# Kernel optimization log

Hardware: AMD Instinct MI355X
Metric: run time of the kernel (lower is better)

## Reference

```python
import jax, jax.numpy as jnp
import numpy as np

H = 2048        # hidden_size
NH = 16         # num heads
QLR = 1536      # q_lora_rank
KVLR = 512      # kv_lora_rank
NOPE = 128      # qk_nope_head_dim
ROPE = 64       # qk_rope_head_dim
VH = 128        # v_head_dim
QHD = NOPE + ROPE
EPS = 1e-6
THETA = 10000.0


def rms_norm(x, w):
    x32 = x.astype(jnp.float32)
    inv = jax.lax.rsqrt(jnp.mean(x32 * x32, axis=-1, keepdims=True) + EPS)
    return (x32 * inv * w.astype(jnp.float32)).astype(x.dtype)


def rotate_half(x):
    h = x.shape[-1] // 2
    return jnp.concatenate([-x[..., h:], x[..., :h]], axis=-1)


def setup_inputs() -> dict:
    key = jax.random.key(0)
    ks = jax.random.split(key, 8)
    s = 0.02
    return {
        "hidden_states": jax.random.normal(ks[0], (1, 2048, H), dtype=jnp.float32),
        "q_a_w": jax.random.normal(ks[1], (QLR, H), dtype=jnp.float32) * s,
        "q_a_ln_w": jnp.ones((QLR,), dtype=jnp.float32),
        "q_b_w": jax.random.normal(ks[2], (NH * QHD, QLR), dtype=jnp.float32) * s,
        "kv_a_w": jax.random.normal(ks[3], (KVLR + ROPE, H), dtype=jnp.float32) * s,
        "kv_a_ln_w": jnp.ones((KVLR,), dtype=jnp.float32),
        "kv_b_w": jax.random.normal(ks[4], (NH * (NOPE + VH), KVLR), dtype=jnp.float32) * s,
        "o_w": jax.random.normal(ks[5], (H, NH * VH), dtype=jnp.float32) * s,
    }


def reference(hidden_states, q_a_w, q_a_ln_w, q_b_w, kv_a_w, kv_a_ln_w, kv_b_w, o_w):
    bsz, q_len, _ = hidden_states.shape
    scale = QHD ** -0.5

    # Q path: low-rank down-proj -> RMSNorm -> up-proj
    q_lat = rms_norm(hidden_states @ q_a_w.T, q_a_ln_w)
    q = (q_lat @ q_b_w.T).reshape(bsz, q_len, NH, QHD).transpose(0, 2, 1, 3)  # [B,H,S,QHD]
    q_nope, q_pe = q[..., :NOPE], q[..., NOPE:]

    # KV path: shared latent + decoupled rope key
    kv_lat_pe = hidden_states @ kv_a_w.T
    kv_lat, k_pe = kv_lat_pe[..., :KVLR], kv_lat_pe[..., KVLR:]
    k_pe = k_pe.reshape(bsz, q_len, 1, ROPE).transpose(0, 2, 1, 3)  # [B,1,S,R]
    kv = (rms_norm(kv_lat, kv_a_ln_w) @ kv_b_w.T).reshape(bsz, q_len, NH, NOPE + VH).transpose(0, 2, 1, 3)
    k_nope, v = kv[..., :NOPE], kv[..., NOPE:]

    # RoPE on decoupled sub-dim
    inv_freq = 1.0 / THETA ** (jnp.arange(0, ROPE, 2, dtype=jnp.float32) / ROPE)
    t = jnp.arange(q_len, dtype=jnp.float32)
    freqs = jnp.outer(t, inv_freq)
    emb = jnp.concatenate([freqs, freqs], axis=-1)
    cos = jnp.cos(emb)[None, None]  # [1,1,S,R]
    sin = jnp.sin(emb)[None, None]
    q_pe = q_pe * cos + rotate_half(q_pe) * sin
    k_pe = k_pe * cos + rotate_half(k_pe) * sin

    qs = jnp.concatenate([q_nope, q_pe], axis=-1)                                   # [B,H,S,QHD]
    ks = jnp.concatenate([k_nope, jnp.broadcast_to(k_pe, (bsz, NH, q_len, ROPE))], axis=-1)

    # causal SDPA
    scores = jnp.einsum('bhqd,bhkd->bhqk', qs, ks) * scale
    mask = jnp.tril(jnp.ones((q_len, q_len), dtype=bool))
    scores = jnp.where(mask[None, None], scores, jnp.finfo(scores.dtype).min)
    p = jax.nn.softmax(scores, axis=-1)
    attn = jnp.einsum('bhqk,bhkd->bhqd', p, v)

    attn = attn.transpose(0, 2, 1, 3).reshape(bsz, q_len, NH * VH)
    return attn @ o_w.T
```

## Files before the change

kernel.cpp:

```cpp
#include <hip/hip_runtime.h>
#include <cstdint>

#define H 2048
#define NH 16
#define QLR 1536
#define KVLR 512
#define NOPE 128
#define ROPED 64
#define VH 128
#define QHD 192
#define SEQ 2048
#define NQH (NH*QHD)
#define NKVC (NH*(NOPE+VH))
#define NOV (NH*VH)
#define KVAW_N (KVLR+ROPED)
#define SCALE_L2E 0.10411755f
#define NSEG 4

typedef __attribute__((ext_vector_type(8))) short short8;
typedef __attribute__((ext_vector_type(4))) short short4v;
typedef __attribute__((ext_vector_type(4))) float floatx4;

__device__ __forceinline__ short f2bf(float x) {
  unsigned u = __builtin_bit_cast(unsigned, x);
  unsigned r = (u + 0x7FFFu + ((u >> 16) & 1u)) >> 16;
  return (short)(unsigned short)r;
}
__device__ __forceinline__ float bf2f(short s) {
  unsigned u = ((unsigned)(unsigned short)s) << 16;
  return __builtin_bit_cast(float, u);
}
__device__ __forceinline__ void g2l16(const void* g, void* l) {
  __builtin_amdgcn_global_load_lds(
      (const __attribute__((address_space(1))) void*)(uintptr_t)(g),
      (__attribute__((address_space(3))) void*)(uintptr_t)(l),
      16, 0, 0);
}


struct CvtArgs {
  const float* src[6];
  short* dst[6];
  int cum[7];
};
__global__ __launch_bounds__(256) void k_cvt_all(CvtArgs a, int total4) {
  int stride = gridDim.x * 256;
  for (int i = blockIdx.x * 256 + threadIdx.x; i < total4; i += stride) {
    int j = 0;
#pragma unroll
    for (int t = 1; t < 6; ++t) j += (i >= a.cum[t]);
    int loc = i - a.cum[j];
    float4 v = ((const float4*)a.src[j])[loc];
    short4v o;
    o.x = f2bf(v.x); o.y = f2bf(v.y); o.z = f2bf(v.z); o.w = f2bf(v.w);
    ((short4v*)a.dst[j])[loc] = o;
  }
}

template<int EPI>
__global__ __launch_bounds__(256) void k_gemm64(
    const short* __restrict__ A, const short* __restrict__ B,
    float* __restrict__ C, float* __restrict__ C2, int N, int K)
{
  __shared__ short As[3][4096];
  __shared__ short Bs[3][2048];
  const int tid = threadIdx.x;
  const int lane = tid & 63;
  const int w = tid >> 6;
  const int wm = w & 1, wn = w >> 1;
  const int quad = lane >> 4, l16 = lane & 15;
  const int m0 = blockIdx.x * 128, n0 = blockIdx.y * 64;
  const int T = K >> 5;

  floatx4 acc[4][2] = {};

  auto issue = [&](int t, int buf) {
#pragma unroll
    for (int i = 0; i < 2; ++i) {
      int c = i*256 + tid;
      int row = c & 127, koct = c >> 7;
      g2l16(A + (size_t)(m0 + row)*K + t*32 + koct*8, As[buf] + (koct*128 + row)*8);
    }
    { int c = tid; int row = c & 63, koct = c >> 6;
      g2l16(B + (size_t)(n0 + row)*K + t*32 + koct*8, Bs[buf] + (koct*64 + row)*8); }
  };

  issue(0, 0);
  issue(1, 1);
  int buf = 0;
  for (int t = 0; t < T; ++t) {
    if (t + 2 < T) {
      int nb = buf - 1; if (nb < 0) nb = 2;
      issue(t + 2, nb);
      asm volatile("s_waitcnt vmcnt(6)" ::: "memory");
    } else if (t + 1 < T) {
      asm volatile("s_waitcnt vmcnt(3)" ::: "memory");
    } else {
      asm volatile("s_waitcnt vmcnt(0)" ::: "memory");
    }
    asm volatile("s_barrier" ::: "memory");
    short8 af[4], bfr[2];
#pragma unroll
    for (int mi = 0; mi < 4; ++mi)
      af[mi] = *(const short8*)(As[buf] + (quad*128 + wm*64 + mi*16 + l16)*8);
#pragma unroll
    for (int ni = 0; ni < 2; ++ni)
      bfr[ni] = *(const short8*)(Bs[buf] + (quad*64 + wn*32 + ni*16 + l16)*8);
#pragma unroll
    for (int mi = 0; mi < 4; ++mi)
#pragma unroll
      for (int ni = 0; ni < 2; ++ni)
        acc[mi][ni] = __builtin_amdgcn_mfma_f32_16x16x32_bf16(af[mi], bfr[ni], acc[mi][ni], 0, 0, 0);
    asm volatile("s_barrier" ::: "memory");
    buf = buf + 1; if (buf > 2) buf = 0;
  }

#pragma unroll
  for (int mi = 0; mi < 4; ++mi) {
#pragma unroll
    for (int ni = 0; ni < 2; ++ni) {
      int col = n0 + wn*32 + ni*16 + l16;
#pragma unroll
      for (int r = 0; r < 4; ++r) {
        int row = m0 + wm*64 + mi*16 + quad*4 + r;
        if (EPI == 0) {
          C[(size_t)row*N + col] = acc[mi][ni][r];
        } else {
          if (col < QLR) C[(size_t)row*QLR + col] = acc[mi][ni][r];
          else           C2[(size_t)row*KVAW_N + (col - QLR)] = acc[mi][ni][r];
        }
      }
    }
  }
}

__global__ __launch_bounds__(256) void k_gemm2(
    const short* __restrict__ qlatn, const short* __restrict__ qbw,
    const short* __restrict__ kvln,  const short* __restrict__ kvbw,
    short* __restrict__ qhm, short* __restrict__ knope, short* __restrict__ vTd)
{
  __shared__ short As[3][4096];
  __shared__ short Bs[3][4096];
  const int tid = threadIdx.x;
  const int lane = tid & 63;
  const int w = tid >> 6;
  const int wm = w & 1, wn = w >> 1;
  const int quad = lane >> 4, l16 = lane & 15;
  int bid = blockIdx.x;
  const short *A, *B; int K, m0, n0; bool isq;
  if (bid < 384) { isq = true;  A = qlatn; B = qbw;  K = QLR;
    m0 = (bid & 15) * 128; n0 = (bid >> 4) * 128; }
  else { int b2 = bid - 384; isq = false; A = kvln; B = kvbw; K = KVLR;
    m0 = (b2 & 15) * 128; n0 = (b2 >> 4) * 128; }
  const int T = K >> 5;

  floatx4 acc[4][4] = {};

  auto issue = [&](int t, int buf) {
#pragma unroll
    for (int i = 0; i < 2; ++i) {
      int c = i*256 + tid;
      int row = c & 127, koct = c >> 7;
      g2l16(A + (size_t)(m0 + row)*K + t*32 + koct*8, As[buf] + (koct*128 + row)*8);
      g2l16(B + (size_t)(n0 + row)*K + t*32 + koct*8, Bs[buf] + (koct*128 + row)*8);
    }
  };

  issue(0, 0);
  issue(1, 1);
  int buf = 0;
  for (int t = 0; t < T; ++t) {
    if (t + 2 < T) {
      int nb = buf - 1; if (nb < 0) nb = 2;
      issue(t + 2, nb);
      asm volatile("s_waitcnt vmcnt(8)" ::: "memory");
    } else if (t + 1 < T) {
      asm volatile("s_waitcnt vmcnt(4)" ::: "memory");
    } else {
      asm volatile("s_waitcnt vmcnt(0)" ::: "memory");
    }
    asm volatile("s_barrier" ::: "memory");
    short8 af[4], bfr[4];
#pragma unroll
    for (int mi = 0; mi < 4; ++mi)
      af[mi] = *(const short8*)(As[buf] + (quad*128 + wm*64 + mi*16 + l16)*8);
#pragma unroll
    for (int ni = 0; ni < 4; ++ni)
      bfr[ni] = *(const short8*)(Bs[buf] + (quad*128 + wn*64 + ni*16 + l16)*8);
#pragma unroll
    for (int mi = 0; mi < 4; ++mi)
#pragma unroll
      for (int ni = 0; ni < 4; ++ni)
        acc[mi][ni] = __builtin_amdgcn_mfma_f32_16x16x32_bf16(af[mi], bfr[ni], acc[mi][ni], 0, 0, 0);
    asm volatile("s_barrier" ::: "memory");
    buf = buf + 1; if (buf > 2) buf = 0;
  }

  const int n064 = n0 + wn * 64;
  if (isq) {
    const int h = n064 / QHD;
    const bool ropew = (n064 % QHD) == 128;
    if (!ropew) {
      const int dbase = n064 - h * QHD;
#pragma unroll
      for (int mi = 0; mi < 4; ++mi) {
        const int qt = (m0 + wm*64 + mi*16) >> 4;
#pragma unroll
        for (int ni = 0; ni < 4; ++ni) {
          int d = dbase + ni*16 + l16;
          size_t tb = ((size_t)(h*128 + qt)*6 + (d>>5))*512
                    + (size_t)(((d>>3)&3)*16)*8 + (d&7);
#pragma unroll
          for (int r = 0; r < 4; ++r)
            qhm[tb + (quad*4 + r)*8] = f2bf(acc[mi][ni][r] * SCALE_L2E);
        }
      }
    } else {
#pragma unroll
      for (int ni = 0; ni < 2; ++ni) {
        int i = ni*16 + l16;
        float fr = powf(10000.0f, -(float)i / 32.0f);
        const int qoff = ((i>>3)*16)*8 + (i&7);
#pragma unroll
        for (int mi = 0; mi < 4; ++mi) {
          const int qt = (m0 + wm*64 + mi*16) >> 4;
          size_t t4 = ((size_t)(h*128 + qt)*6 + 4)*512 + qoff;
#pragma unroll
          for (int r = 0; r < 4; ++r) {
            int row = m0 + wm*64 + mi*16 + quad*4 + r;
            float ang = (float)row * fr;
            float cv, sv; __sincosf(ang, &sv, &cv);
            float x1 = acc[mi][ni][r], x2 = acc[mi][ni+2][r];
            qhm[t4 + (quad*4 + r)*8]       = f2bf((x1*cv - x2*sv) * SCALE_L2E);
            qhm[t4 + 512 + (quad*4 + r)*8] = f2bf((x2*cv + x1*sv) * SCALE_L2E);
          }
        }
      }
    }
  } else {
    const bool isv = (n064 & 128) != 0;
    if (!isv) {
#pragma unroll
      for (int mi = 0; mi < 4; ++mi) {
        const int kt = (m0 + wm*64 + mi*16) >> 4;
#pragma unroll
        for (int ni = 0; ni < 4; ++ni) {
          int col = n064 + ni*16 + l16;
          int hh = col >> 8, d = col & 127;
          size_t tb = ((size_t)(hh*128 + kt)*4 + (d>>5))*512
                    + (size_t)(((d>>3)&3)*16)*8 + (d&7);
#pragma unroll
          for (int r = 0; r < 4; ++r)
            knope[tb + (quad*4 + r)*8] = f2bf(acc[mi][ni][r]);
        }
      }
    } else {
#pragma unroll
      for (int mi = 0; mi < 4; ++mi) {
        const int row0 = m0 + wm*64 + mi*16 + quad*4;
        const int kb = row0 >> 5;
        const int voff = (((row0>>3)&3)*16)*8 + (row0 & 7);
#pragma unroll
        for (int ni = 0; ni < 4; ++ni) {
          int col = n064 + ni*16 + l16;
          int hh = col >> 8, dv = (col & 255) - 128;
          short4v pk;
          pk.x = f2bf(acc[mi][ni][0]); pk.y = f2bf(acc[mi][ni][1]);
          pk.z = f2bf(acc[mi][ni][2]); pk.w = f2bf(acc[mi][ni][3]);
          *(short4v*)(vTd + ((size_t)(hh*8 + (dv>>4))*64 + kb)*512
                          + voff + (dv & 15)*8) = pk;
        }
      }
    }
  }
}

__global__ __launch_bounds__(256) void k_rms2(
    const float* __restrict__ qlat, const float* __restrict__ q_a_ln,
    short* __restrict__ qlatn,
    const float* __restrict__ kvlp, const float* __restrict__ kv_a_ln,
    short* __restrict__ kvln, short* __restrict__ kpe)
{
  int b = blockIdx.x;
  __shared__ float red[4];
  if (b < SEQ) {
    int row = b;
    const float* xr = qlat + (size_t)row * QLR;
    float s = 0.f;
    for (int i = threadIdx.x; i < QLR; i += 256) { float v = xr[i]; s += v*v; }
#pragma unroll
    for (int off = 1; off < 64; off <<= 1) s += __shfl_xor(s, off);
    if ((threadIdx.x & 63) == 0) red[threadIdx.x >> 6] = s;
    __syncthreads();
    float inv = rsqrtf((red[0]+red[1]+red[2]+red[3]) / (float)QLR + 1e-6f);
    for (int i = threadIdx.x; i < QLR; i += 256)
      qlatn[(size_t)row * QLR + i] = f2bf(xr[i] * inv * q_a_ln[i]);
  } else {
    int row = b - SEQ;
    const float* xr = kvlp + (size_t)row * KVAW_N;
    float s = 0.f;
    for (int i = threadIdx.x; i < KVLR; i += 256) { float v = xr[i]; s += v*v; }
#pragma unroll
    for (int off = 1; off < 64; off <<= 1) s += __shfl_xor(s, off);
    if ((threadIdx.x & 63) == 0) red[threadIdx.x >> 6] = s;
    __syncthreads();
    float inv = rsqrtf((red[0]+red[1]+red[2]+red[3]) / (float)KVLR + 1e-6f);
    for (int i = threadIdx.x; i < KVLR; i += 256)
      kvln[(size_t)row * KVLR + i] = f2bf(xr[i] * inv * kv_a_ln[i]);
    if (threadIdx.x < 32) {
      int i = threadIdx.x;
      float ang = (float)row * powf(10000.0f, -(float)i / 32.0f);
      float cv, sv; __sincosf(ang, &sv, &cv);
      float x1 = xr[KVLR + i], x2 = xr[KVLR + 32 + i];
      size_t t0 = (size_t)((row >> 4) * 2) * 512
                + (size_t)(((i >> 3) * 16) + (row & 15)) * 8 + (i & 7);
      kpe[t0]       = f2bf(x1*cv - x2*sv);
      kpe[t0 + 512] = f2bf(x2*cv + x1*sv);
    }
  }
}

__global__ __launch_bounds__(256) void k_attn7(
    const short* __restrict__ qhm,
    const short* __restrict__ knope,
    const short* __restrict__ kpe,
    const short* __restrict__ vT,
    short* __restrict__ Opart,
    float2* __restrict__ mlb)
{
  __shared__ short Pl[4][32 * 136];
  const int tid = threadIdx.x;
  const int lane = tid & 63, w = tid >> 6;
  const int quad = lane >> 4, l16 = lane & 15;
  const int b = blockIdx.x;
  const int h = b & 15;
  const int r = (39 - (b >> 4)) * 4 + w;
  int qw, seg;
  if (r < 16)      { qw = r; seg = 0; }
  else if (r < 48) { int x = r - 16; qw = 16 + (x >> 1); seg = x & 1; }
  else if (r < 96) { int x = r - 48; int d3 = x / 3; qw = 32 + d3; seg = x - 3*d3; }
  else             { int x = r - 96; qw = 48 + (x >> 2); seg = x & 3; }
  const int qws = qw * 32;
  const int tc = (qw + 4) >> 2;
  const int cs = seg * 4;
  const int cend = (tc < cs + 4) ? tc : (cs + 4);
  short* Plw = Pl[w];

  const short* qbase = qhm   + (size_t)h * (128*6*512);
  const short* kbase = knope + (size_t)h * (128*4*512);
  const short* vbase = vT    + (size_t)h * (8*64*512);

  const int qt0 = qws >> 4;
  short8 qf[2][6];
#pragma unroll
  for (int nt = 0; nt < 2; ++nt)
#pragma unroll
    for (int ks = 0; ks < 6; ++ks)
      qf[nt][ks] = *(const short8*)(qbase + ((size_t)(qt0 + nt)*6 + ks)*512 + lane*8);

  floatx4 oacc[8][2] = {};
  float m_i[2] = {-1e30f, -1e30f}, l_i[2] = {0.f, 0.f};

  for (int kc = cs; kc < cend; ++kc) {
    const int kv0 = kc * 128;

    floatx4 s[8][2] = {};
#pragma unroll
    for (int mt = 0; mt < 8; ++mt) {
      const int kt = (kv0 >> 4) + mt;
      const short* kr  = kbase + (size_t)kt * 2048 + lane*8;
      const short* rr2 = kpe   + (size_t)kt * 1024 + lane*8;
      short8 kf0 = *(const short8*)(kr);
      short8 kf1 = *(const short8*)(kr + 512);
      short8 kf2 = *(const short8*)(kr + 1024);
      short8 kf3 = *(const short8*)(kr + 1536);
      short8 kf4 = *(const short8*)(rr2);
      short8 kf5 = *(const short8*)(rr2 + 512);
      s[mt][0] = __builtin_amdgcn_mfma_f32_16x16x32_bf16(kf0, qf[0][0], s[mt][0], 0, 0, 0);
      s[mt][1] = __builtin_amdgcn_mfma_f32_16x16x32_bf16(kf0, qf[1][0], s[mt][1], 0, 0, 0);
      s[mt][0] = __builtin_amdgcn_mfma_f32_16x16x32_bf16(kf1, qf[0][1], s[mt][0], 0, 0, 0);
      s[mt][1] = __builtin_amdgcn_mfma_f32_16x16x32_bf16(kf1, qf[1][1], s[mt][1], 0, 0, 0);
      s[mt][0] = __builtin_amdgcn_mfma_f32_16x16x32_bf16(kf2, qf[0][2], s[mt][0], 0, 0, 0);
      s[mt][1] = __builtin_amdgcn_mfma_f32_16x16x32_bf16(kf2, qf[1][2], s[mt][1], 0, 0, 0);
      s[mt][0] = __builtin_amdgcn_mfma_f32_16x16x32_bf16(kf3, qf[0][3], s[mt][0], 0, 0, 0);
      s[mt][1] = __builtin_amdgcn_mfma_f32_16x16x32_bf16(kf3, qf[1][3], s[mt][1], 0, 0, 0);
      s[mt][0] = __builtin_amdgcn_mfma_f32_16x16x32_bf16(kf4, qf[0][4], s[mt][0], 0, 0, 0);
      s[mt][1] = __builtin_amdgcn_mfma_f32_16x16x32_bf16(kf4, qf[1][4], s[mt][1], 0, 0, 0);
      s[mt][0] = __builtin_amdgcn_mfma_f32_16x16x32_bf16(kf5, qf[0][5], s[mt][0], 0, 0, 0);
      s[mt][1] = __builtin_amdgcn_mfma_f32_16x16x32_bf16(kf5, qf[1][5], s[mt][1], 0, 0, 0);
    }

    const bool diag = (kv0 + 128 > qws);
#pragma unroll
    for (int nt = 0; nt < 2; ++nt) {
      const int qg = qws + nt*16 + l16;
      float mx = -1e30f;
#pragma unroll
      for (int mt = 0; mt < 8; ++mt)
#pragma unroll
        for (int rr = 0; rr < 4; ++rr) {
          float v = s[mt][nt][rr];
          if (diag) {
            int kvg = kv0 + mt*16 + quad*4 + rr;
            v = (kvg <= qg) ? v : -1e30f;
            s[mt][nt][rr] = v;
          }
          mx = fmaxf(mx, v);
        }
      mx = fmaxf(mx, __shfl_xor(mx, 16));
      mx = fmaxf(mx, __shfl_xor(mx, 32));
      float mnew = fmaxf(m_i[nt], mx);
      float alpha = exp2f(m_i[nt] - mnew);
      m_i[nt] = mnew;
      float ssum = 0.f;
#pragma unroll
      for (int mt = 0; mt < 8; ++mt) {
        float p0 = exp2f(s[mt][nt][0] - mnew);
        float p1 = exp2f(s[mt][nt][1] - mnew);
        float p2 = exp2f(s[mt][nt][2] - mnew);
        float p3 = exp2f(s[mt][nt][3] - mnew);
        ssum += (p0 + p1) + (p2 + p3);
        short4v pk; pk.x = f2bf(p0); pk.y = f2bf(p1); pk.z = f2bf(p2); pk.w = f2bf(p3);
        *(short4v*)(Plw + (nt*16 + l16)*136 + mt*16 + quad*4) = pk;
      }
      ssum += __shfl_xor(ssum, 16);
      ssum += __shfl_xor(ssum, 32);
      l_i[nt] = l_i[nt] * alpha + ssum;
#pragma unroll
      for (int dt = 0; dt < 8; ++dt)
#pragma unroll
        for (int rr = 0; rr < 4; ++rr) oacc[dt][nt][rr] *= alpha;
    }

#pragma unroll
    for (int sl = 0; sl < 4; ++sl) {
      const int kb = (kv0 >> 5) + sl;
      short8 pf0 = *(const short8*)(Plw + l16*136 + sl*32 + quad*8);
      short8 pf1 = *(const short8*)(Plw + (16 + l16)*136 + sl*32 + quad*8);
#pragma unroll
      for (int dt = 0; dt < 8; ++dt) {
        short8 vf = *(const short8*)(vbase + ((size_t)dt*64 + kb)*512 + lane*8);
        oacc[dt][0] = __builtin_amdgcn_mfma_f32_16x16x32_bf16(vf, pf0, oacc[dt][0], 0, 0, 0);
        oacc[dt][1] = __builtin_amdgcn_mfma_f32_16x16x32_bf16(vf, pf1, oacc[dt][1], 0, 0, 0);
      }
    }
  }

#pragma unroll
  for (int nt = 0; nt < 2; ++nt) {
    float inv = (l_i[nt] > 0.f) ? 1.f / l_i[nt] : 0.f;
    int q = qws + nt*16 + l16;
    if (quad == 0)
      mlb[((size_t)seg * SEQ + q) * NH + h] = make_float2(m_i[nt], l_i[nt]);
#pragma unroll
    for (int dt = 0; dt < 8; ++dt) {
      short4v pk;
      pk.x = f2bf(oacc[dt][nt][0] * inv);
      pk.y = f2bf(oacc[dt][nt][1] * inv);
      pk.z = f2bf(oacc[dt][nt][2] * inv);
      pk.w = f2bf(oacc[dt][nt][3] * inv);
      *(short4v*)(Opart + ((size_t)seg * SEQ + q) * NOV + h * VH + dt*16 + quad*4) = pk;
    }
  }
}

__global__ __launch_bounds__(256) void k_comb(
    const short* __restrict__ Opart, const float2* __restrict__ mlb,
    short* __restrict__ ob)
{
  int q = blockIdx.x;
  int hd0 = threadIdx.x * 8;
  int h = hd0 >> 7;
  int nact = (q >> 9) + 1;
  float2 mlv[NSEG];
  float M = -1e30f;
  for (int s = 0; s < nact; ++s) {
    mlv[s] = mlb[((size_t)s * SEQ + q) * NH + h];
    M = fmaxf(M, mlv[s].x);
  }
  float wgt[NSEG]; float L = 0.f;
  for (int s = 0; s < nact; ++s) {
    wgt[s] = mlv[s].y * exp2f(mlv[s].x - M);
    L += wgt[s];
  }
  float invL = 1.0f / L;
  float acc[8] = {};
  for (int s = 0; s < nact; ++s) {
    short8 o = *(const short8*)(Opart + ((size_t)s * SEQ + q) * NOV + hd0);
    float ws = wgt[s] * invL;
#pragma unroll
    for (int j = 0; j < 8; ++j) acc[j] += ws * bf2f(o[j]);
  }
  short8 rr;
#pragma unroll
  for (int j = 0; j < 8; ++j) rr[j] = f2bf(acc[j]);
  *(short8*)(ob + (size_t)q * NOV + hd0) = rr;
}

extern "C" void kernel_launch(void* const* d_in, const int* in_sizes, int n_in,
                              void* d_out, int out_size, void* d_ws, size_t ws_size,
                              hipStream_t stream) {
  const float* hs      = (const float*)d_in[0];
  const float* q_a_w   = (const float*)d_in[1];
  const float* q_a_ln  = (const float*)d_in[2];
  const float* q_b_w   = (const float*)d_in[3];
  const float* kv_a_w  = (const float*)d_in[4];
  const float* kv_a_ln = (const float*)d_in[5];
  const float* kv_b_w  = (const float*)d_in[6];
  const float* o_w     = (const float*)d_in[7];
  float* out = (float*)d_out;

  char* ws = (char*)d_ws;
  size_t off = 0;
  auto alloc = [&](size_t bytes) {
    void* p = ws + off;
    off += (bytes + 255) & ~(size_t)255;
    return p;
  };
  const size_t MB = 1u << 20;
  short* hs_b   = (short*)alloc((size_t)SEQ * H * 2);
  short* wab    = (short*)alloc((size_t)(QLR + KVAW_N) * H * 2);
  short* qbw_b  = (short*)alloc((size_t)NQH * QLR * 2);
  short* kvbw_b = (short*)alloc((size_t)NKVC * KVLR * 2);
  short* ow_b   = (short*)alloc((size_t)H * NOV * 2);
  short* qhm    = (short*)alloc((size_t)NH * SEQ * QHD * 2);
  short* kpeb   = (short*)alloc((size_t)SEQ * ROPED * 2);
  short* knope  = (short*)alloc((size_t)NH * SEQ * NOPE * 2);
  short* vT     = (short*)alloc((size_t)NH * VH * SEQ * 2);
  short* attnb  = (short*)alloc((size_t)SEQ * NOV * 2);
  char* R = (char*)alloc(36 * MB);
  float* qlat  = (float*)R;
  short* qlatn = (short*)(R + 13 * MB);
  short* kvln  = (short*)(R + 20 * MB);
  float* kvlp  = (float*)(R + 24 * MB);
  short* Opart = (short*)R;
  float2* mlb  = (float2*)(R + 34 * MB);

  CvtArgs ca;
  ca.src[0] = hs;     ca.dst[0] = hs_b;
  ca.src[1] = q_a_w;  ca.dst[1] = wab;
  ca.src[2] = kv_a_w; ca.dst[2] = wab + (size_t)QLR * H;
  ca.src[3] = q_b_w;  ca.dst[3] = qbw_b;
  ca.src[4] = kv_b_w; ca.dst[4] = kvbw_b;
  ca.src[5] = o_w;    ca.dst[5] = ow_b;
  int sizes4[6] = { SEQ*H/4, QLR*H/4, KVAW_N*H/4, NQH*QLR/4, NKVC*KVLR/4, H*NOV/4 };
  ca.cum[0] = 0;
  for (int i = 0; i < 6; ++i) ca.cum[i+1] = ca.cum[i] + sizes4[i];
  k_cvt_all<<<2048, 256, 0, stream>>>(ca, ca.cum[6]);

  k_gemm64<1><<<dim3(SEQ/128, (QLR + KVAW_N)/64), 256, 0, stream>>>(
      hs_b, wab, qlat, kvlp, QLR + KVAW_N, H);
  k_rms2<<<2*SEQ, 256, 0, stream>>>(qlat, q_a_ln, qlatn, kvlp, kv_a_ln, kvln, kpeb);
  k_gemm2<<<896, 256, 0, stream>>>(qlatn, qbw_b, kvln, kvbw_b, qhm, knope, vT);
  k_attn7<<<640, 256, 0, stream>>>(qhm, knope, kpeb, vT, Opart, mlb);
  k_comb<<<SEQ, 256, 0, stream>>>(Opart, mlb, attnb);
  k_gemm64<0><<<dim3(SEQ/128, H/64), 256, 0, stream>>>(
      attnb, ow_b, out, nullptr, H, NOV);
}
```

Baseline: 445.4 us.

## Stage K/V tiles in double-buffered LDS shared across waves in attention

The attention kernel now loads K-nope, K-rope and V tiles for each 64-key chunk cooperatively into double-buffered shared memory, using async global-to-LDS copies. The next chunk is prefetched while the current one is computed. Previously each wave read K/V directly from global memory. The change also regroups work so all four waves of a block share one 128-row query block, assigned through a constant task table. Chunk size drops from 128 to 64 keys, which adds barriers and vmcnt waits in exchange for reusing each loaded tile across four waves and hiding load latency. The LDS footprint grows substantially, which may reduce occupancy.

```diff
diff --git a/kernel.cpp b/kernel.cpp
--- a/kernel.cpp
+++ b/kernel.cpp
@@ -320,7 +320,12 @@
   }
 }
 
-__global__ __launch_bounds__(256) void k_attn7(
+__device__ __constant__ unsigned char g_task[40] = {
+  60,61,62,63, 56,57,58, 52,53,54, 48,49,50, 44,45,46,
+  40,41, 36,37, 32,33, 28,29, 24, 20, 16, 12,
+  59,42,25,8, 55,38,21,4, 51,34,17,0 };
+
+__global__ __launch_bounds__(256) void k_attn8(
     const short* __restrict__ qhm,
     const short* __restrict__ knope,
     const short* __restrict__ kpe,
@@ -328,22 +333,19 @@
     short* __restrict__ Opart,
     float2* __restrict__ mlb)
 {
-  __shared__ short Pl[4][32 * 136];
+  __shared__ short Ls[2][20480];
+  __shared__ short Pl[4][32 * 72];
   const int tid = threadIdx.x;
   const int lane = tid & 63, w = tid >> 6;
   const int quad = lane >> 4, l16 = lane & 15;
   const int b = blockIdx.x;
   const int h = b & 15;
-  const int r = (39 - (b >> 4)) * 4 + w;
-  int qw, seg;
-  if (r < 16)      { qw = r; seg = 0; }
-  else if (r < 48) { int x = r - 16; qw = 16 + (x >> 1); seg = x & 1; }
-  else if (r < 96) { int x = r - 48; int d3 = x / 3; qw = 32 + d3; seg = x - 3*d3; }
-  else             { int x = r - 96; qw = 48 + (x >> 2); seg = x & 3; }
-  const int qws = qw * 32;
-  const int tc = (qw + 4) >> 2;
-  const int cs = seg * 4;
-  const int cend = (tc < cs + 4) ? tc : (cs + 4);
+  const int qs2 = g_task[b >> 4];
+  const int qb = qs2 >> 2, seg = qs2 & 3;
+  const int cs = seg * 8;
+  const int cend0 = 2 * qb + 2;
+  const int cend = (cend0 < cs + 8) ? cend0 : (cs + 8);
+  const int qws = qb * 128 + w * 32;
   short* Plw = Pl[w];
 
   const short* qbase = qhm   + (size_t)h * (128*6*512);
@@ -358,24 +360,48 @@
     for (int ks = 0; ks < 6; ++ks)
       qf[nt][ks] = *(const short8*)(qbase + ((size_t)(qt0 + nt)*6 + ks)*512 + lane*8);
 
+  auto issue = [&](int kc, int buf) {
+    short* L = &Ls[buf][0];
+    const short* ksrc = kbase + (size_t)kc * 8192;
+    const short* psrc = kpe   + (size_t)kc * 4096;
+#pragma unroll
+    for (int i = 0; i < 4; ++i)
+      g2l16(ksrc + (i*256 + tid)*8, L + (i*256 + tid)*8);
+#pragma unroll
+    for (int i = 0; i < 2; ++i)
+      g2l16(psrc + (i*256 + tid)*8, L + 8192 + (i*256 + tid)*8);
+#pragma unroll
+    for (int i = 0; i < 4; ++i) {
+      int uv = i*256 + tid;
+      int dt = uv >> 7, wi = uv & 127;
+      g2l16(vbase + ((size_t)(dt*64 + kc*2))*512 + wi*8, L + 12288 + uv*8);
+    }
+  };
+
+  issue(cs, 0);
+  if (cs + 1 < cend) issue(cs + 1, 1);
+
   floatx4 oacc[8][2] = {};
   float m_i[2] = {-1e30f, -1e30f}, l_i[2] = {0.f, 0.f};
 
   for (int kc = cs; kc < cend; ++kc) {
-    const int kv0 = kc * 128;
-
-    floatx4 s[8][2] = {};
-#pragma unroll
-    for (int mt = 0; mt < 8; ++mt) {
-      const int kt = (kv0 >> 4) + mt;
-      const short* kr  = kbase + (size_t)kt * 2048 + lane*8;
-      const short* rr2 = kpe   + (size_t)kt * 1024 + lane*8;
+    if (kc + 1 < cend) asm volatile("s_waitcnt vmcnt(10)" ::: "memory");
+    else               asm volatile("s_waitcnt vmcnt(0)" ::: "memory");
+    asm volatile("s_barrier" ::: "memory");
+    const short* Lb = &Ls[kc & 1][0];
+    const int kv0 = kc * 64;
+
+    floatx4 s[4][2] = {};
+#pragma unroll
+    for (int mt = 0; mt < 4; ++mt) {
+      const short* kr = Lb + mt*2048 + lane*8;
+      const short* pr = Lb + 8192 + mt*1024 + lane*8;
       short8 kf0 = *(const short8*)(kr);
       short8 kf1 = *(const short8*)(kr + 512);
       short8 kf2 = *(const short8*)(kr + 1024);
       short8 kf3 = *(const short8*)(kr + 1536);
-      short8 kf4 = *(const short8*)(rr2);
-      short8 kf5 = *(const short8*)(rr2 + 512);
+      short8 kf4 = *(const short8*)(pr);
+      short8 kf5 = *(const short8*)(pr + 512);
       s[mt][0] = __builtin_amdgcn_mfma_f32_16x16x32_bf16(kf0, qf[0][0], s[mt][0], 0, 0, 0);
       s[mt][1] = __builtin_amdgcn_mfma_f32_16x16x32_bf16(kf0, qf[1][0], s[mt][1], 0, 0, 0);
       s[mt][0] = __builtin_amdgcn_mfma_f32_16x16x32_bf16(kf1, qf[0][1], s[mt][0], 0, 0, 0);
@@ -390,13 +416,13 @@
       s[mt][1] = __builtin_amdgcn_mfma_f32_16x16x32_bf16(kf5, qf[1][5], s[mt][1], 0, 0, 0);
     }
 
-    const bool diag = (kv0 + 128 > qws);
+    const bool diag = (kv0 + 64 > qws);
 #pragma unroll
     for (int nt = 0; nt < 2; ++nt) {
       const int qg = qws + nt*16 + l16;
       float mx = -1e30f;
 #pragma unroll
-      for (int mt = 0; mt < 8; ++mt)
+      for (int mt = 0; mt < 4; ++mt)
 #pragma unroll
         for (int rr = 0; rr < 4; ++rr) {
           float v = s[mt][nt][rr];
@@ -414,14 +440,14 @@
       m_i[nt] = mnew;
       float ssum = 0.f;
 #pragma unroll
-      for (int mt = 0; mt < 8; ++mt) {
+      for (int mt = 0; mt < 4; ++mt) {
         float p0 = exp2f(s[mt][nt][0] - mnew);
         float p1 = exp2f(s[mt][nt][1] - mnew);
         float p2 = exp2f(s[mt][nt][2] - mnew);
         float p3 = exp2f(s[mt][nt][3] - mnew);
         ssum += (p0 + p1) + (p2 + p3);
         short4v pk; pk.x = f2bf(p0); pk.y = f2bf(p1); pk.z = f2bf(p2); pk.w = f2bf(p3);
-        *(short4v*)(Plw + (nt*16 + l16)*136 + mt*16 + quad*4) = pk;
+        *(short4v*)(Plw + (nt*16 + l16)*72 + mt*16 + quad*4) = pk;
       }
       ssum += __shfl_xor(ssum, 16);
       ssum += __shfl_xor(ssum, 32);
@@ -433,17 +459,19 @@
     }
 
 #pragma unroll
-    for (int sl = 0; sl < 4; ++sl) {
-      const int kb = (kv0 >> 5) + sl;
-      short8 pf0 = *(const short8*)(Plw + l16*136 + sl*32 + quad*8);
-      short8 pf1 = *(const short8*)(Plw + (16 + l16)*136 + sl*32 + quad*8);
+    for (int sl = 0; sl < 2; ++sl) {
+      short8 pf0 = *(const short8*)(Plw + l16*72 + sl*32 + quad*8);
+      short8 pf1 = *(const short8*)(Plw + (16 + l16)*72 + sl*32 + quad*8);
 #pragma unroll
       for (int dt = 0; dt < 8; ++dt) {
-        short8 vf = *(const short8*)(vbase + ((size_t)dt*64 + kb)*512 + lane*8);
+        short8 vf = *(const short8*)(Lb + 12288 + (dt*2 + sl)*512 + lane*8);
         oacc[dt][0] = __builtin_amdgcn_mfma_f32_16x16x32_bf16(vf, pf0, oacc[dt][0], 0, 0, 0);
         oacc[dt][1] = __builtin_amdgcn_mfma_f32_16x16x32_bf16(vf, pf1, oacc[dt][1], 0, 0, 0);
       }
     }
+
+    asm volatile("s_barrier" ::: "memory");
+    if (kc + 2 < cend) issue(kc + 2, kc & 1);
   }
 
 #pragma unroll
@@ -552,7 +580,7 @@
       hs_b, wab, qlat, kvlp, QLR + KVAW_N, H);
   k_rms2<<<2*SEQ, 256, 0, stream>>>(qlat, q_a_ln, qlatn, kvlp, kv_a_ln, kvln, kpeb);
   k_gemm2<<<896, 256, 0, stream>>>(qlatn, qbw_b, kvln, kvbw_b, qhm, knope, vT);
-  k_attn7<<<640, 256, 0, stream>>>(qhm, knope, kpeb, vT, Opart, mlb);
+  k_attn8<<<640, 256, 0, stream>>>(qhm, knope, kpeb, vT, Opart, mlb);
   k_comb<<<SEQ, 256, 0, stream>>>(Opart, mlb, attnb);
   k_gemm64<0><<<dim3(SEQ/128, H/64), 256, 0, stream>>>(
       attnb, ow_b, out, nullptr, H, NOV);
```

After: 407.8 us. -8.4%, faster.
